# Kernel tuning notes

Measured on AMD Instinct MI355X. Metric: run time of the kernel, lower is better.

Reference implementation:

```python
import jax, jax.numpy as jnp
import numpy as np

EPS = 1e-9


def _pairwise_sqdist(x1, x2):
    # x1: (B,n,3), x2: (B,m,3) -> (B,n,m) squared euclidean distances
    s1 = jnp.sum(x1 * x1, axis=-1)
    s2 = jnp.sum(x2 * x2, axis=-1)
    cross = jnp.einsum('bnd,bmd->bnm', x1, x2)
    return jnp.maximum(s1[:, :, None] + s2[:, None, :] - 2.0 * cross, 0.0)


def _approxmatch(x1, x2):
    # Faithful port of the approxmatch CUDA kernel (Fan et al. EMD approx).
    B, n, _ = x1.shape
    m = x2.shape[1]
    if n >= m:
        multiL, multiR = 1.0, float(n // m)   # integer division as in CUDA
    else:
        multiL, multiR = float(m // n), 1.0
    dist = _pairwise_sqdist(x1, x2)  # (B,n,m)
    # j = 7 .. -1 -> level = -4^j ; j = -2 -> level = 0  (10 sweeps total)
    levels = jnp.concatenate([
        -(4.0 ** jnp.arange(7, -2, -1, dtype=jnp.float32)),
        jnp.zeros((1,), jnp.float32)])
    match0 = jnp.zeros((B, n, m), jnp.float32)
    remainL0 = jnp.full((B, n), multiL, jnp.float32)
    remainR0 = jnp.full((B, m), multiR, jnp.float32)

    def body(carry, level):
        match, remainL, remainR = carry
        e = jnp.exp(level * dist)                              # (B,n,m)
        suml = EPS + jnp.einsum('bnm,bm->bn', e, remainR)
        ratioL = remainL / suml                                # (B,n)
        sumr = remainR * jnp.einsum('bnm,bn->bm', e, ratioL)   # (B,m)
        consumption = jnp.minimum(remainR / (sumr + EPS), 1.0)
        ratioR = consumption * remainR                         # (B,m)
        remainR = jnp.maximum(0.0, remainR - sumr)
        w = e * ratioL[:, :, None] * ratioR[:, None, :]        # flow k->l
        match = match + w
        remainL = jnp.maximum(0.0, remainL - jnp.sum(w, axis=-1))
        return (match, remainL, remainR), None

    (match, _, _), _ = jax.lax.scan(body, (match0, remainL0, remainR0), levels)
    return match, dist


def setup_inputs() -> dict:
    key = jax.random.key(0)
    k1, k2 = jax.random.split(key)
    B, N = 4, 4096
    xyz1 = jax.random.normal(k1, (B, 3, N), dtype=jnp.float32)
    xyz2 = jax.random.normal(k2, (B, 3, N), dtype=jnp.float32)
    return {"xyz1": xyz1, "xyz2": xyz2}


def reference(xyz1, xyz2):
    # transpose=True: BCN -> BNC
    x1 = jnp.transpose(xyz1, (0, 2, 1))
    x2 = jnp.transpose(xyz2, (0, 2, 1))
    match, dist = _approxmatch(x1, x2)
    d = jnp.sqrt(jnp.maximum(dist, 1e-20))
    cost = jnp.sum(match * d, axis=(1, 2))            # (B,)
    emd = cost / min(x1.shape[1], x2.shape[1])
    return jnp.mean(emd)                               # reduce_mean=True
```

## Files before the change

### kernel.cpp

```cpp
#include <hip/hip_runtime.h>


#define NPTS 4096
#define BATCH 4
#define EMD_EPS 1e-9f
#define TILE 1024
#define RPW 4
#define THREADS 256
#define RPB 16
#define NBLK (NPTS / RPB)

__device__ __forceinline__ float fexp2(float x) {
#if __has_builtin(__builtin_amdgcn_exp2f)
    return __builtin_amdgcn_exp2f(x);
#else
    return exp2f(x);
#endif
}
__device__ __forceinline__ float fsqrt(float x) {
#if __has_builtin(__builtin_amdgcn_sqrtf)
    return __builtin_amdgcn_sqrtf(x);
#else
    return __sqrtf(x);
#endif
}

__device__ __forceinline__ float wave_reduce(float v) {
    v += __shfl_xor(v, 32);
    v += __shfl_xor(v, 16);
    v += __shfl_xor(v, 8);
    v += __shfl_xor(v, 4);
    v += __shfl_xor(v, 2);
    v += __shfl_xor(v, 1);
    return v;
}

__global__ void k_init(float* __restrict__ remainL, float* __restrict__ remainR,
                       float* __restrict__ cost_part) {
    int i = blockIdx.x * blockDim.x + threadIdx.x;
    if (i < BATCH * NPTS) {
        remainL[i] = 1.0f;
        remainR[i] = 1.0f;
    }
    if (i < BATCH * NBLK) cost_part[i] = 0.0f;
}

__global__ __launch_bounds__(THREADS, 2) void k_ratioL0(
        const float* __restrict__ xyz1, const float* __restrict__ xyz2,
        float* __restrict__ ratioL, float ls2) {
    const int b = blockIdx.y;
    const int tid = threadIdx.x;
    const int wave = tid >> 6;
    const int lane = tid & 63;
    const int row0 = blockIdx.x * RPB + wave * RPW;

    const float* x1 = xyz1 + b * 3 * NPTS;
    const float* x2 = xyz2 + b * 3 * NPTS;
    const float2* x2x = (const float2*)(x2);
    const float2* x2y = (const float2*)(x2 + NPTS);
    const float2* x2z = (const float2*)(x2 + 2 * NPTS);

    float px[RPW], py[RPW], pz[RPW];
    float2 acc[RPW];
#pragma unroll
    for (int r = 0; r < RPW; ++r) {
        px[r] = x1[row0 + r];
        py[r] = x1[NPTS + row0 + r];
        pz[r] = x1[2 * NPTS + row0 + r];
        acc[r] = make_float2(0.0f, 0.0f);
    }
    __shared__ float4 sA[TILE / 2];
    __shared__ float2 sZ[TILE / 2];

    for (int c0 = 0; c0 < NPTS; c0 += TILE) {
        __syncthreads();
        for (int i = tid; i < TILE / 2; i += THREADS) {
            int e = c0 / 2 + i;
            float2 xx = x2x[e], yy = x2y[e];
            sA[i] = make_float4(xx.x, xx.y, yy.x, yy.y);
            sZ[i] = x2z[e];
        }
        __syncthreads();
#pragma unroll 2
        for (int j = 0; j < TILE / 128; ++j) {
            float4 a = sA[lane + 64 * j];
            float2 z = sZ[lane + 64 * j];
#pragma unroll
            for (int r = 0; r < RPW; ++r) {
                float dx0 = px[r] - a.x, dx1 = px[r] - a.y;
                float dy0 = py[r] - a.z, dy1 = py[r] - a.w;
                float dz0 = pz[r] - z.x, dz1 = pz[r] - z.y;
                float d0 = fmaf(dx0, dx0, fmaf(dy0, dy0, dz0 * dz0));
                float d1 = fmaf(dx1, dx1, fmaf(dy1, dy1, dz1 * dz1));
                acc[r].x += fexp2(ls2 * d0);
                acc[r].y += fexp2(ls2 * d1);
            }
        }
    }
#pragma unroll
    for (int r = 0; r < RPW; ++r) {
        float s = wave_reduce(acc[r].x + acc[r].y);
        if (lane == 0)
            ratioL[b * NPTS + row0 + r] = 1.0f / (EMD_EPS + s);
    }
}

__global__ __launch_bounds__(THREADS, 2) void k_ratioR(
        const float* __restrict__ xyz1, const float* __restrict__ xyz2,
        const float* __restrict__ ratioL, float* __restrict__ ratioR,
        float* __restrict__ remainR, float ls2) {
    const int b = blockIdx.y;
    const int tid = threadIdx.x;
    const int wave = tid >> 6;
    const int lane = tid & 63;
    const int col0 = blockIdx.x * RPB + wave * RPW;

    const float* x1 = xyz1 + b * 3 * NPTS;
    const float* x2 = xyz2 + b * 3 * NPTS;
    const float2* x1x = (const float2*)(x1);
    const float2* x1y = (const float2*)(x1 + NPTS);
    const float2* x1z = (const float2*)(x1 + 2 * NPTS);
    const float2* wLv = (const float2*)(ratioL + b * NPTS);

    float px[RPW], py[RPW], pz[RPW];
    float2 acc[RPW];
#pragma unroll
    for (int r = 0; r < RPW; ++r) {
        px[r] = x2[col0 + r];
        py[r] = x2[NPTS + col0 + r];
        pz[r] = x2[2 * NPTS + col0 + r];
        acc[r] = make_float2(0.0f, 0.0f);
    }
    __shared__ float4 sA[TILE / 2];
    __shared__ float4 sB[TILE / 2];

    for (int c0 = 0; c0 < NPTS; c0 += TILE) {
        __syncthreads();
        for (int i = tid; i < TILE / 2; i += THREADS) {
            int e = c0 / 2 + i;
            float2 xx = x1x[e], yy = x1y[e], zz = x1z[e], ww = wLv[e];
            sA[i] = make_float4(xx.x, xx.y, yy.x, yy.y);
            sB[i] = make_float4(zz.x, zz.y, ww.x, ww.y);
        }
        __syncthreads();
#pragma unroll 2
        for (int j = 0; j < TILE / 128; ++j) {
            float4 a = sA[lane + 64 * j];
            float4 bq = sB[lane + 64 * j];
#pragma unroll
            for (int r = 0; r < RPW; ++r) {
                float dx0 = px[r] - a.x, dx1 = px[r] - a.y;
                float dy0 = py[r] - a.z, dy1 = py[r] - a.w;
                float dz0 = pz[r] - bq.x, dz1 = pz[r] - bq.y;
                float d0 = fmaf(dx0, dx0, fmaf(dy0, dy0, dz0 * dz0));
                float d1 = fmaf(dx1, dx1, fmaf(dy1, dy1, dz1 * dz1));
                acc[r].x = fmaf(fexp2(ls2 * d0), bq.z, acc[r].x);
                acc[r].y = fmaf(fexp2(ls2 * d1), bq.w, acc[r].y);
            }
        }
    }
#pragma unroll
    for (int r = 0; r < RPW; ++r) {
        float s = wave_reduce(acc[r].x + acc[r].y);
        if (lane == 0) {
            int idx = b * NPTS + col0 + r;
            float rv = remainR[idx];
            float sumr = rv * s;
            float cons = fminf(rv / (sumr + EMD_EPS), 1.0f);
            ratioR[idx] = cons * rv;
            remainR[idx] = fmaxf(0.0f, rv - sumr);
        }
    }
}

template <bool SQ>
__global__ __launch_bounds__(THREADS, 2) void k_cost_fused(
        const float* __restrict__ xyz1, const float* __restrict__ xyz2,
        float* __restrict__ ratioL, const float* __restrict__ ratioR,
        float* __restrict__ remainL, const float* __restrict__ remainR,
        float* __restrict__ cost_part, float ls2, float ls2n) {
    const int b = blockIdx.y;
    const int tid = threadIdx.x;
    const int wave = tid >> 6;
    const int lane = tid & 63;
    const int row0 = blockIdx.x * RPB + wave * RPW;

    const float* x1 = xyz1 + b * 3 * NPTS;
    const float* x2 = xyz2 + b * 3 * NPTS;
    const float2* x2x = (const float2*)(x2);
    const float2* x2y = (const float2*)(x2 + NPTS);
    const float2* x2z = (const float2*)(x2 + 2 * NPTS);
    const float2* wRv = (const float2*)(ratioR + b * NPTS);
    const float2* w2v = (const float2*)(remainR + b * NPTS);

    float px[RPW], py[RPW], pz[RPW];
    float2 acc_a[RPW], acc_c[RPW], acc_s[RPW];
#pragma unroll
    for (int r = 0; r < RPW; ++r) {
        px[r] = x1[row0 + r];
        py[r] = x1[NPTS + row0 + r];
        pz[r] = x1[2 * NPTS + row0 + r];
        acc_a[r] = make_float2(0.0f, 0.0f);
        acc_c[r] = make_float2(0.0f, 0.0f);
        acc_s[r] = make_float2(0.0f, 0.0f);
    }
    __shared__ float4 sA[TILE / 2];
    __shared__ float4 sB[TILE / 2];
    __shared__ float2 sC[TILE / 2];
    __shared__ float s_cost[THREADS / 64];

    for (int c0 = 0; c0 < NPTS; c0 += TILE) {
        __syncthreads();
        for (int i = tid; i < TILE / 2; i += THREADS) {
            int e = c0 / 2 + i;
            float2 xx = x2x[e], yy = x2y[e], zz = x2z[e], wr = wRv[e];
            sA[i] = make_float4(xx.x, xx.y, yy.x, yy.y);
            sB[i] = make_float4(zz.x, zz.y, wr.x, wr.y);
            sC[i] = w2v[e];
        }
        __syncthreads();
#pragma unroll 2
        for (int j = 0; j < TILE / 128; ++j) {
            float4 a = sA[lane + 64 * j];
            float4 bq = sB[lane + 64 * j];
            float2 c = sC[lane + 64 * j];
#pragma unroll
            for (int r = 0; r < RPW; ++r) {
                float dx0 = px[r] - a.x, dx1 = px[r] - a.y;
                float dy0 = py[r] - a.z, dy1 = py[r] - a.w;
                float dz0 = pz[r] - bq.x, dz1 = pz[r] - bq.y;
                float d0 = fmaf(dx0, dx0, fmaf(dy0, dy0, dz0 * dz0));
                float d1 = fmaf(dx1, dx1, fmaf(dy1, dy1, dz1 * dz1));
                float er0, er1;
                if (SQ) {
                    float e20 = fexp2(ls2n * d0);
                    float e21 = fexp2(ls2n * d1);
                    acc_s[r].x = fmaf(e20, c.x, acc_s[r].x);
                    acc_s[r].y = fmaf(e21, c.y, acc_s[r].y);
                    float e40 = e20 * e20, e41 = e21 * e21;
                    er0 = (e40 * e40) * bq.z;
                    er1 = (e41 * e41) * bq.w;
                } else {
                    er0 = fexp2(ls2 * d0) * bq.z;
                    er1 = fexp2(ls2 * d1) * bq.w;
                    acc_s[r].x += c.x;
                    acc_s[r].y += c.y;
                }
                acc_a[r].x += er0;
                acc_a[r].y += er1;
                acc_c[r].x = fmaf(er0, fsqrt(d0), acc_c[r].x);
                acc_c[r].y = fmaf(er1, fsqrt(d1), acc_c[r].y);
            }
        }
    }
    float wcost = 0.0f;
#pragma unroll
    for (int r = 0; r < RPW; ++r) {
        float sa = wave_reduce(acc_a[r].x + acc_a[r].y);
        float sc = wave_reduce(acc_c[r].x + acc_c[r].y);
        float ss = wave_reduce(acc_s[r].x + acc_s[r].y);
        if (lane == 0) {
            int idx = b * NPTS + row0 + r;
            float rl = ratioL[idx];
            float rem = fmaxf(0.0f, remainL[idx] - rl * sa);
            remainL[idx] = rem;
            ratioL[idx] = rem / (EMD_EPS + ss);
            wcost = fmaf(rl, sc, wcost);
        }
    }
    if (lane == 0) s_cost[wave] = wcost;
    __syncthreads();
    if (tid == 0) {
        float t = s_cost[0] + s_cost[1] + s_cost[2] + s_cost[3];
        cost_part[b * NBLK + blockIdx.x] += t;
    }
}

__global__ void k_sum_ratioL(const float* __restrict__ ratioL, float* __restrict__ S_L) {
    const int b = blockIdx.x;
    const int tid = threadIdx.x;
    float s = 0.0f;
    for (int i = tid; i < NPTS; i += 256) s += ratioL[b * NPTS + i];
    s = wave_reduce(s);
    __shared__ float sw[4];
    if ((tid & 63) == 0) sw[tid >> 6] = s;
    __syncthreads();
    if (tid == 0) S_L[b] = sw[0] + sw[1] + sw[2] + sw[3];
}

__global__ void k_ratioR_l0(const float* __restrict__ remainR,
                            const float* __restrict__ S_L,
                            float* __restrict__ ratioR) {
    int i = blockIdx.x * blockDim.x + threadIdx.x;
    int b = i >> 12;
    float rv = remainR[i];
    float sumr = rv * S_L[b];
    float cons = fminf(rv / (sumr + EMD_EPS), 1.0f);
    ratioR[i] = cons * rv;
}

__global__ __launch_bounds__(THREADS, 2) void k_cost_l0(
        const float* __restrict__ xyz1, const float* __restrict__ xyz2,
        const float* __restrict__ ratioL, const float* __restrict__ ratioR,
        float* __restrict__ cost_part) {
    const int b = blockIdx.y;
    const int tid = threadIdx.x;
    const int wave = tid >> 6;
    const int lane = tid & 63;
    const int row0 = blockIdx.x * RPB + wave * RPW;

    const float* x1 = xyz1 + b * 3 * NPTS;
    const float* x2 = xyz2 + b * 3 * NPTS;
    const float2* x2x = (const float2*)(x2);
    const float2* x2y = (const float2*)(x2 + NPTS);
    const float2* x2z = (const float2*)(x2 + 2 * NPTS);
    const float2* wRv = (const float2*)(ratioR + b * NPTS);

    float px[RPW], py[RPW], pz[RPW];
    float2 acc_c[RPW];
#pragma unroll
    for (int r = 0; r < RPW; ++r) {
        px[r] = x1[row0 + r];
        py[r] = x1[NPTS + row0 + r];
        pz[r] = x1[2 * NPTS + row0 + r];
        acc_c[r] = make_float2(0.0f, 0.0f);
    }
    __shared__ float4 sA[TILE / 2];
    __shared__ float4 sB[TILE / 2];
    __shared__ float s_cost[THREADS / 64];

    for (int c0 = 0; c0 < NPTS; c0 += TILE) {
        __syncthreads();
        for (int i = tid; i < TILE / 2; i += THREADS) {
            int e = c0 / 2 + i;
            float2 xx = x2x[e], yy = x2y[e], zz = x2z[e], wr = wRv[e];
            sA[i] = make_float4(xx.x, xx.y, yy.x, yy.y);
            sB[i] = make_float4(zz.x, zz.y, wr.x, wr.y);
        }
        __syncthreads();
#pragma unroll 2
        for (int j = 0; j < TILE / 128; ++j) {
            float4 a = sA[lane + 64 * j];
            float4 bq = sB[lane + 64 * j];
#pragma unroll
            for (int r = 0; r < RPW; ++r) {
                float dx0 = px[r] - a.x, dx1 = px[r] - a.y;
                float dy0 = py[r] - a.z, dy1 = py[r] - a.w;
                float dz0 = pz[r] - bq.x, dz1 = pz[r] - bq.y;
                float d0 = fmaf(dx0, dx0, fmaf(dy0, dy0, dz0 * dz0));
                float d1 = fmaf(dx1, dx1, fmaf(dy1, dy1, dz1 * dz1));
                acc_c[r].x = fmaf(bq.z, fsqrt(d0), acc_c[r].x);
                acc_c[r].y = fmaf(bq.w, fsqrt(d1), acc_c[r].y);
            }
        }
    }
    float wcost = 0.0f;
#pragma unroll
    for (int r = 0; r < RPW; ++r) {
        float sc = wave_reduce(acc_c[r].x + acc_c[r].y);
        if (lane == 0)
            wcost = fmaf(ratioL[b * NPTS + row0 + r], sc, wcost);
    }
    if (lane == 0) s_cost[wave] = wcost;
    __syncthreads();
    if (tid == 0) {
        float t = s_cost[0] + s_cost[1] + s_cost[2] + s_cost[3];
        cost_part[b * NBLK + blockIdx.x] += t;
    }
}

__global__ void k_final(const float* __restrict__ cost_part, float* __restrict__ out) {
    const int tid = threadIdx.x;
    float s = 0.0f;
    for (int i = tid; i < BATCH * NBLK; i += 256) s += cost_part[i];
    s = wave_reduce(s);
    __shared__ float sw[4];
    if ((tid & 63) == 0) sw[tid >> 6] = s;
    __syncthreads();
    if (tid == 0) out[0] = (sw[0] + sw[1] + sw[2] + sw[3]) / ((float)NPTS * (float)BATCH);
}

extern "C" void kernel_launch(void* const* d_in, const int* in_sizes, int n_in,
                              void* d_out, int out_size, void* d_ws, size_t ws_size,
                              hipStream_t stream) {
    const float* xyz1 = (const float*)d_in[0];
    const float* xyz2 = (const float*)d_in[1];
    float* out = (float*)d_out;

    float* ws = (float*)d_ws;
    float* remainL  = ws;
    float* remainR  = ws + 1 * BATCH * NPTS;
    float* ratioL   = ws + 2 * BATCH * NPTS;
    float* ratioR   = ws + 3 * BATCH * NPTS;
    float* cost_part = ws + 4 * BATCH * NPTS;
    float* S_L      = cost_part + BATCH * NBLK;

    static const float levels[10] = {
        -16384.0f, -4096.0f, -1024.0f, -256.0f, -64.0f,
        -16.0f, -4.0f, -1.0f, -0.25f, 0.0f};
    float ls2[10];
    for (int t = 0; t < 10; ++t)
        ls2[t] = (float)(levels[t] * 1.4426950408889634);

    dim3 grid(NBLK, BATCH);

    k_init<<<(BATCH * NPTS + 255) / 256, 256, 0, stream>>>(remainL, remainR, cost_part);
    k_ratioL0<<<grid, THREADS, 0, stream>>>(xyz1, xyz2, ratioL, ls2[0]);
    for (int t = 0; t < 8; ++t) {
        k_ratioR<<<grid, THREADS, 0, stream>>>(xyz1, xyz2, ratioL, ratioR, remainR, ls2[t]);
        k_cost_fused<true><<<grid, THREADS, 0, stream>>>(xyz1, xyz2, ratioL, ratioR,
                                                         remainL, remainR, cost_part,
                                                         ls2[t], ls2[t + 1]);
    }
    k_ratioR<<<grid, THREADS, 0, stream>>>(xyz1, xyz2, ratioL, ratioR, remainR, ls2[8]);
    k_cost_fused<false><<<grid, THREADS, 0, stream>>>(xyz1, xyz2, ratioL, ratioR,
                                                      remainL, remainR, cost_part,
                                                      ls2[8], 0.0f);
    k_sum_ratioL<<<BATCH, 256, 0, stream>>>(ratioL, S_L);
    k_ratioR_l0<<<(BATCH * NPTS) / 256, 256, 0, stream>>>(remainR, S_L, ratioR);
    k_cost_l0<<<grid, THREADS, 0, stream>>>(xyz1, xyz2, ratioL, ratioR, cost_part);
    k_final<<<1, 256, 0, stream>>>(cost_part, out);
}
```

Baseline: 575.0 us.

## Morton-sort points and skip far tile pairs via bounding-box distance culling

Adds a per-batch Morton-code counting sort of both point clouds and per-128-point tile bounding boxes. Each wave then skips tiles whose minimum squared distance makes exp(level*d) negligible, below about 2^-160, which removes most exp work at the steep early levels. It also folds the init and ratioR_l0 kernels into neighbouring kernels. The culling is approximate and drops tiny contributions. The sort quantizes over a fixed [-5,5] range, but out-of-range points are clamped, so correctness does not depend on that range.

```diff
diff --git a/kernel.cpp b/kernel.cpp
--- a/kernel.cpp
+++ b/kernel.cpp
@@ -9,6 +9,7 @@
 #define THREADS 256
 #define RPB 16
 #define NBLK (NPTS / RPB)
+#define NTILE 32
 
 __device__ __forceinline__ float fexp2(float x) {
 #if __has_builtin(__builtin_amdgcn_exp2f)
@@ -35,27 +36,122 @@
     return v;
 }
 
-__global__ void k_init(float* __restrict__ remainL, float* __restrict__ remainR,
-                       float* __restrict__ cost_part) {
-    int i = blockIdx.x * blockDim.x + threadIdx.x;
-    if (i < BATCH * NPTS) {
-        remainL[i] = 1.0f;
-        remainR[i] = 1.0f;
-    }
-    if (i < BATCH * NBLK) cost_part[i] = 0.0f;
-}
+__device__ __forceinline__ unsigned spread4(unsigned v) {
+    return (v & 1u) | ((v & 2u) << 2) | ((v & 4u) << 4) | ((v & 8u) << 6);
+}
+
+__global__ __launch_bounds__(1024) void k_sort(
+        const float* __restrict__ xyz1, const float* __restrict__ xyz2,
+        float* __restrict__ x1s, float* __restrict__ x2s) {
+    const int side = blockIdx.x, b = blockIdx.y;
+    const float* src = (side ? xyz2 : xyz1) + b * 3 * NPTS;
+    float* dst = (side ? x2s : x1s) + b * 3 * NPTS;
+    const int tid = threadIdx.x;
+    const int lane = tid & 63, wave = tid >> 6;
+
+    __shared__ unsigned hist[4096];
+    __shared__ unsigned short keys[4096];
+    __shared__ unsigned warr[16];
+
+    for (int i = tid; i < 4096; i += 1024) hist[i] = 0u;
+    __syncthreads();
+    for (int i = tid; i < NPTS; i += 1024) {
+        float x = src[i], y = src[NPTS + i], z = src[2 * NPTS + i];
+        unsigned qx = (unsigned)fminf(fmaxf((x + 5.0f) * 1.6f, 0.0f), 15.0f);
+        unsigned qy = (unsigned)fminf(fmaxf((y + 5.0f) * 1.6f, 0.0f), 15.0f);
+        unsigned qz = (unsigned)fminf(fmaxf((z + 5.0f) * 1.6f, 0.0f), 15.0f);
+        unsigned key = spread4(qx) | (spread4(qy) << 1) | (spread4(qz) << 2);
+        keys[i] = (unsigned short)key;
+        atomicAdd(&hist[key], 1u);
+    }
+    __syncthreads();
+    const int base = tid * 4;
+    unsigned h0 = hist[base], h1 = hist[base + 1], h2 = hist[base + 2], h3 = hist[base + 3];
+    unsigned st = h0 + h1 + h2 + h3;
+    unsigned v = st;
+    for (int d = 1; d < 64; d <<= 1) {
+        unsigned u = __shfl_up(v, d);
+        if (lane >= d) v += u;
+    }
+    if (lane == 63) warr[wave] = v;
+    __syncthreads();
+    if (tid == 0) {
+        unsigned run = 0;
+        for (int w = 0; w < 16; ++w) { unsigned t = warr[w]; warr[w] = run; run += t; }
+    }
+    __syncthreads();
+    unsigned off = warr[wave] + (v - st);
+    hist[base] = off;
+    hist[base + 1] = off + h0;
+    hist[base + 2] = off + h0 + h1;
+    hist[base + 3] = off + h0 + h1 + h2;
+    __syncthreads();
+    for (int i = tid; i < NPTS; i += 1024) {
+        unsigned k = keys[i];
+        unsigned pos = atomicAdd(&hist[k], 1u);
+        dst[pos] = src[i];
+        dst[NPTS + pos] = src[NPTS + i];
+        dst[2 * NPTS + pos] = src[2 * NPTS + i];
+    }
+}
+
+__global__ void k_bbox(const float* __restrict__ x1s, const float* __restrict__ x2s,
+                       float* __restrict__ bb1, float* __restrict__ bb2) {
+    const int tile = blockIdx.x, b = blockIdx.y, side = blockIdx.z;
+    const float* src = (side ? x2s : x1s) + b * 3 * NPTS + tile * 128;
+    float* out = (side ? bb2 : bb1) + (b * NTILE + tile) * 8;
+    const int lane = threadIdx.x;
+    float mnx = 1e30f, mny = 1e30f, mnz = 1e30f;
+    float mxx = -1e30f, mxy = -1e30f, mxz = -1e30f;
+    for (int i = lane; i < 128; i += 64) {
+        float x = src[i], y = src[NPTS + i], z = src[2 * NPTS + i];
+        mnx = fminf(mnx, x); mny = fminf(mny, y); mnz = fminf(mnz, z);
+        mxx = fmaxf(mxx, x); mxy = fmaxf(mxy, y); mxz = fmaxf(mxz, z);
+    }
+    for (int d = 32; d; d >>= 1) {
+        mnx = fminf(mnx, __shfl_xor(mnx, d));
+        mny = fminf(mny, __shfl_xor(mny, d));
+        mnz = fminf(mnz, __shfl_xor(mnz, d));
+        mxx = fmaxf(mxx, __shfl_xor(mxx, d));
+        mxy = fmaxf(mxy, __shfl_xor(mxy, d));
+        mxz = fmaxf(mxz, __shfl_xor(mxz, d));
+    }
+    if (lane == 0) {
+        out[0] = mnx; out[1] = mny; out[2] = mnz;
+        out[3] = mxx; out[4] = mxy; out[5] = mxz;
+    }
+}
+
+#define BB_TEST(ti)                                                          \
+    float bmnx = sBB[(ti) * 8 + 0], bmny = sBB[(ti) * 8 + 1],                \
+          bmnz = sBB[(ti) * 8 + 2], bmxx = sBB[(ti) * 8 + 3],                \
+          bmxy = sBB[(ti) * 8 + 4], bmxz = sBB[(ti) * 8 + 5];                \
+    float ddx = fmaxf(0.0f, fmaxf(bmnx - gmxx, gmnx - bmxx));                \
+    float ddy = fmaxf(0.0f, fmaxf(bmny - gmxy, gmny - bmxy));                \
+    float ddz = fmaxf(0.0f, fmaxf(bmnz - gmxz, gmnz - bmxz));                \
+    float md2 = fmaf(ddx, ddx, fmaf(ddy, ddy, ddz * ddz));
+
+#define WAVE_BBOX()                                                          \
+    float gmnx = fminf(fminf(px[0], px[1]), fminf(px[2], px[3]));            \
+    float gmxx = fmaxf(fmaxf(px[0], px[1]), fmaxf(px[2], px[3]));            \
+    float gmny = fminf(fminf(py[0], py[1]), fminf(py[2], py[3]));            \
+    float gmxy = fmaxf(fmaxf(py[0], py[1]), fmaxf(py[2], py[3]));            \
+    float gmnz = fminf(fminf(pz[0], pz[1]), fminf(pz[2], pz[3]));            \
+    float gmxz = fmaxf(fmaxf(pz[0], pz[1]), fmaxf(pz[2], pz[3]));
 
 __global__ __launch_bounds__(THREADS, 2) void k_ratioL0(
-        const float* __restrict__ xyz1, const float* __restrict__ xyz2,
-        float* __restrict__ ratioL, float ls2) {
+        const float* __restrict__ x1s, const float* __restrict__ x2s,
+        const float* __restrict__ bb2,
+        float* __restrict__ ratioL, float* __restrict__ remainL,
+        float* __restrict__ remainR, float ls2, float thresh) {
     const int b = blockIdx.y;
     const int tid = threadIdx.x;
     const int wave = tid >> 6;
     const int lane = tid & 63;
     const int row0 = blockIdx.x * RPB + wave * RPW;
 
-    const float* x1 = xyz1 + b * 3 * NPTS;
-    const float* x2 = xyz2 + b * 3 * NPTS;
+    const float* x1 = x1s + b * 3 * NPTS;
+    const float* x2 = x2s + b * 3 * NPTS;
     const float2* x2x = (const float2*)(x2);
     const float2* x2y = (const float2*)(x2 + NPTS);
     const float2* x2z = (const float2*)(x2 + 2 * NPTS);
@@ -69,8 +165,11 @@
         pz[r] = x1[2 * NPTS + row0 + r];
         acc[r] = make_float2(0.0f, 0.0f);
     }
+    WAVE_BBOX();
     __shared__ float4 sA[TILE / 2];
     __shared__ float2 sZ[TILE / 2];
+    __shared__ float sBB[NTILE * 8];
+    if (tid < NTILE * 8) sBB[tid] = bb2[b * NTILE * 8 + tid];
 
     for (int c0 = 0; c0 < NPTS; c0 += TILE) {
         __syncthreads();
@@ -83,40 +182,48 @@
         __syncthreads();
 #pragma unroll 2
         for (int j = 0; j < TILE / 128; ++j) {
-            float4 a = sA[lane + 64 * j];
-            float2 z = sZ[lane + 64 * j];
-#pragma unroll
-            for (int r = 0; r < RPW; ++r) {
-                float dx0 = px[r] - a.x, dx1 = px[r] - a.y;
-                float dy0 = py[r] - a.z, dy1 = py[r] - a.w;
-                float dz0 = pz[r] - z.x, dz1 = pz[r] - z.y;
-                float d0 = fmaf(dx0, dx0, fmaf(dy0, dy0, dz0 * dz0));
-                float d1 = fmaf(dx1, dx1, fmaf(dy1, dy1, dz1 * dz1));
-                acc[r].x += fexp2(ls2 * d0);
-                acc[r].y += fexp2(ls2 * d1);
+            BB_TEST((c0 >> 7) + j);
+            if (md2 < thresh) {
+                float4 a = sA[lane + 64 * j];
+                float2 z = sZ[lane + 64 * j];
+#pragma unroll
+                for (int r = 0; r < RPW; ++r) {
+                    float dx0 = px[r] - a.x, dx1 = px[r] - a.y;
+                    float dy0 = py[r] - a.z, dy1 = py[r] - a.w;
+                    float dz0 = pz[r] - z.x, dz1 = pz[r] - z.y;
+                    float d0 = fmaf(dx0, dx0, fmaf(dy0, dy0, dz0 * dz0));
+                    float d1 = fmaf(dx1, dx1, fmaf(dy1, dy1, dz1 * dz1));
+                    acc[r].x += fexp2(ls2 * d0);
+                    acc[r].y += fexp2(ls2 * d1);
+                }
             }
         }
     }
 #pragma unroll
     for (int r = 0; r < RPW; ++r) {
         float s = wave_reduce(acc[r].x + acc[r].y);
-        if (lane == 0)
-            ratioL[b * NPTS + row0 + r] = 1.0f / (EMD_EPS + s);
+        if (lane == 0) {
+            int idx = b * NPTS + row0 + r;
+            ratioL[idx] = 1.0f / (EMD_EPS + s);
+            remainL[idx] = 1.0f;
+            remainR[idx] = 1.0f;
+        }
     }
 }
 
 __global__ __launch_bounds__(THREADS, 2) void k_ratioR(
-        const float* __restrict__ xyz1, const float* __restrict__ xyz2,
+        const float* __restrict__ x1s, const float* __restrict__ x2s,
+        const float* __restrict__ bb1,
         const float* __restrict__ ratioL, float* __restrict__ ratioR,
-        float* __restrict__ remainR, float ls2) {
+        float* __restrict__ remainR, float ls2, float thresh) {
     const int b = blockIdx.y;
     const int tid = threadIdx.x;
     const int wave = tid >> 6;
     const int lane = tid & 63;
     const int col0 = blockIdx.x * RPB + wave * RPW;
 
-    const float* x1 = xyz1 + b * 3 * NPTS;
-    const float* x2 = xyz2 + b * 3 * NPTS;
+    const float* x1 = x1s + b * 3 * NPTS;
+    const float* x2 = x2s + b * 3 * NPTS;
     const float2* x1x = (const float2*)(x1);
     const float2* x1y = (const float2*)(x1 + NPTS);
     const float2* x1z = (const float2*)(x1 + 2 * NPTS);
@@ -131,8 +238,11 @@
         pz[r] = x2[2 * NPTS + col0 + r];
         acc[r] = make_float2(0.0f, 0.0f);
     }
+    WAVE_BBOX();
     __shared__ float4 sA[TILE / 2];
     __shared__ float4 sB[TILE / 2];
+    __shared__ float sBB[NTILE * 8];
+    if (tid < NTILE * 8) sBB[tid] = bb1[b * NTILE * 8 + tid];
 
     for (int c0 = 0; c0 < NPTS; c0 += TILE) {
         __syncthreads();
@@ -145,17 +255,20 @@
         __syncthreads();
 #pragma unroll 2
         for (int j = 0; j < TILE / 128; ++j) {
-            float4 a = sA[lane + 64 * j];
-            float4 bq = sB[lane + 64 * j];
-#pragma unroll
-            for (int r = 0; r < RPW; ++r) {
-                float dx0 = px[r] - a.x, dx1 = px[r] - a.y;
-                float dy0 = py[r] - a.z, dy1 = py[r] - a.w;
-                float dz0 = pz[r] - bq.x, dz1 = pz[r] - bq.y;
-                float d0 = fmaf(dx0, dx0, fmaf(dy0, dy0, dz0 * dz0));
-                float d1 = fmaf(dx1, dx1, fmaf(dy1, dy1, dz1 * dz1));
-                acc[r].x = fmaf(fexp2(ls2 * d0), bq.z, acc[r].x);
-                acc[r].y = fmaf(fexp2(ls2 * d1), bq.w, acc[r].y);
+            BB_TEST((c0 >> 7) + j);
+            if (md2 < thresh) {
+                float4 a = sA[lane + 64 * j];
+                float4 bq = sB[lane + 64 * j];
+#pragma unroll
+                for (int r = 0; r < RPW; ++r) {
+                    float dx0 = px[r] - a.x, dx1 = px[r] - a.y;
+                    float dy0 = py[r] - a.z, dy1 = py[r] - a.w;
+                    float dz0 = pz[r] - bq.x, dz1 = pz[r] - bq.y;
+                    float d0 = fmaf(dx0, dx0, fmaf(dy0, dy0, dz0 * dz0));
+                    float d1 = fmaf(dx1, dx1, fmaf(dy1, dy1, dz1 * dz1));
+                    acc[r].x = fmaf(fexp2(ls2 * d0), bq.z, acc[r].x);
+                    acc[r].y = fmaf(fexp2(ls2 * d1), bq.w, acc[r].y);
+                }
             }
         }
     }
@@ -175,18 +288,20 @@
 
 template <bool SQ>
 __global__ __launch_bounds__(THREADS, 2) void k_cost_fused(
-        const float* __restrict__ xyz1, const float* __restrict__ xyz2,
+        const float* __restrict__ x1s, const float* __restrict__ x2s,
+        const float* __restrict__ bb2,
         float* __restrict__ ratioL, const float* __restrict__ ratioR,
         float* __restrict__ remainL, const float* __restrict__ remainR,
-        float* __restrict__ cost_part, float ls2, float ls2n) {
+        float* __restrict__ cost_part, float ls2, float ls2n, float thresh,
+        int initCost) {
     const int b = blockIdx.y;
     const int tid = threadIdx.x;
     const int wave = tid >> 6;
     const int lane = tid & 63;
     const int row0 = blockIdx.x * RPB + wave * RPW;
 
-    const float* x1 = xyz1 + b * 3 * NPTS;
-    const float* x2 = xyz2 + b * 3 * NPTS;
+    const float* x1 = x1s + b * 3 * NPTS;
+    const float* x2 = x2s + b * 3 * NPTS;
     const float2* x2x = (const float2*)(x2);
     const float2* x2y = (const float2*)(x2 + NPTS);
     const float2* x2z = (const float2*)(x2 + 2 * NPTS);
@@ -204,10 +319,13 @@
         acc_c[r] = make_float2(0.0f, 0.0f);
         acc_s[r] = make_float2(0.0f, 0.0f);
     }
+    WAVE_BBOX();
     __shared__ float4 sA[TILE / 2];
     __shared__ float4 sB[TILE / 2];
     __shared__ float2 sC[TILE / 2];
+    __shared__ float sBB[NTILE * 8];
     __shared__ float s_cost[THREADS / 64];
+    if (tid < NTILE * 8) sBB[tid] = bb2[b * NTILE * 8 + tid];
 
     for (int c0 = 0; c0 < NPTS; c0 += TILE) {
         __syncthreads();
@@ -221,35 +339,39 @@
         __syncthreads();
 #pragma unroll 2
         for (int j = 0; j < TILE / 128; ++j) {
-            float4 a = sA[lane + 64 * j];
-            float4 bq = sB[lane + 64 * j];
-            float2 c = sC[lane + 64 * j];
-#pragma unroll
-            for (int r = 0; r < RPW; ++r) {
-                float dx0 = px[r] - a.x, dx1 = px[r] - a.y;
-                float dy0 = py[r] - a.z, dy1 = py[r] - a.w;
-                float dz0 = pz[r] - bq.x, dz1 = pz[r] - bq.y;
-                float d0 = fmaf(dx0, dx0, fmaf(dy0, dy0, dz0 * dz0));
-                float d1 = fmaf(dx1, dx1, fmaf(dy1, dy1, dz1 * dz1));
-                float er0, er1;
-                if (SQ) {
-                    float e20 = fexp2(ls2n * d0);
-                    float e21 = fexp2(ls2n * d1);
-                    acc_s[r].x = fmaf(e20, c.x, acc_s[r].x);
-                    acc_s[r].y = fmaf(e21, c.y, acc_s[r].y);
-                    float e40 = e20 * e20, e41 = e21 * e21;
-                    er0 = (e40 * e40) * bq.z;
-                    er1 = (e41 * e41) * bq.w;
-                } else {
-                    er0 = fexp2(ls2 * d0) * bq.z;
-                    er1 = fexp2(ls2 * d1) * bq.w;
-                    acc_s[r].x += c.x;
-                    acc_s[r].y += c.y;
+            BB_TEST((c0 >> 7) + j);
+            if (md2 < thresh) {
+                float4 a = sA[lane + 64 * j];
+                float4 bq = sB[lane + 64 * j];
+                float2 c = sC[lane + 64 * j];
+#pragma unroll
+                for (int r = 0; r < RPW; ++r) {
+                    float dx0 = px[r] - a.x, dx1 = px[r] - a.y;
+                    float dy0 = py[r] - a.z, dy1 = py[r] - a.w;
+                    float dz0 = pz[r] - bq.x, dz1 = pz[r] - bq.y;
+                    float d0 = fmaf(dx0, dx0, fmaf(dy0, dy0, dz0 * dz0));
+                    float d1 = fmaf(dx1, dx1, fmaf(dy1, dy1, dz1 * dz1));
+                    float er0, er1;
+                    if (SQ) {
+                        float e20 = fexp2(ls2n * d0);
+                        float e21 = fexp2(ls2n * d1);
+                        acc_s[r].x = fmaf(e20, c.x, acc_s[r].x);
+                        acc_s[r].y = fmaf(e21, c.y, acc_s[r].y);
+                        float e40 = e20 * e20, e41 = e21 * e21;
+                        er0 = (e40 * e40) * bq.z;
+                        er1 = (e41 * e41) * bq.w;
+                    } else {
+                        er0 = fexp2(ls2 * d0) * bq.z;
+                        er1 = fexp2(ls2 * d1) * bq.w;
+                        acc_s[r].x += c.x;
+                        acc_s[r].y += c.y;
+                    }
+                    acc_a[r].x += er0;
+                    acc_a[r].y += er1;
+                    acc_c[r].x = fmaf(er0, fsqrt(d0), acc_c[r].x);
+                    acc_c[r].y = fmaf(er1, fsqrt(d1), acc_c[r].y);
                 }
-                acc_a[r].x += er0;
-                acc_a[r].y += er1;
-                acc_c[r].x = fmaf(er0, fsqrt(d0), acc_c[r].x);
-                acc_c[r].y = fmaf(er1, fsqrt(d1), acc_c[r].y);
+            } else if (!SQ) {
             }
         }
     }
@@ -272,7 +394,8 @@
     __syncthreads();
     if (tid == 0) {
         float t = s_cost[0] + s_cost[1] + s_cost[2] + s_cost[3];
-        cost_part[b * NBLK + blockIdx.x] += t;
+        int ci = b * NBLK + blockIdx.x;
+        cost_part[ci] = (initCost ? t : cost_part[ci] + t);
     }
 }
 
@@ -288,33 +411,23 @@
     if (tid == 0) S_L[b] = sw[0] + sw[1] + sw[2] + sw[3];
 }
 
-__global__ void k_ratioR_l0(const float* __restrict__ remainR,
-                            const float* __restrict__ S_L,
-                            float* __restrict__ ratioR) {
-    int i = blockIdx.x * blockDim.x + threadIdx.x;
-    int b = i >> 12;
-    float rv = remainR[i];
-    float sumr = rv * S_L[b];
-    float cons = fminf(rv / (sumr + EMD_EPS), 1.0f);
-    ratioR[i] = cons * rv;
-}
-
 __global__ __launch_bounds__(THREADS, 2) void k_cost_l0(
-        const float* __restrict__ xyz1, const float* __restrict__ xyz2,
-        const float* __restrict__ ratioL, const float* __restrict__ ratioR,
-        float* __restrict__ cost_part) {
+        const float* __restrict__ x1s, const float* __restrict__ x2s,
+        const float* __restrict__ ratioL, const float* __restrict__ remainR,
+        const float* __restrict__ S_L, float* __restrict__ cost_part) {
     const int b = blockIdx.y;
     const int tid = threadIdx.x;
     const int wave = tid >> 6;
     const int lane = tid & 63;
     const int row0 = blockIdx.x * RPB + wave * RPW;
-
-    const float* x1 = xyz1 + b * 3 * NPTS;
-    const float* x2 = xyz2 + b * 3 * NPTS;
+    const float sL = S_L[b];
+
+    const float* x1 = x1s + b * 3 * NPTS;
+    const float* x2 = x2s + b * 3 * NPTS;
     const float2* x2x = (const float2*)(x2);
     const float2* x2y = (const float2*)(x2 + NPTS);
     const float2* x2z = (const float2*)(x2 + 2 * NPTS);
-    const float2* wRv = (const float2*)(ratioR + b * NPTS);
+    const float2* wRv = (const float2*)(remainR + b * NPTS);
 
     float px[RPW], py[RPW], pz[RPW];
     float2 acc_c[RPW];
@@ -333,9 +446,11 @@
         __syncthreads();
         for (int i = tid; i < TILE / 2; i += THREADS) {
             int e = c0 / 2 + i;
-            float2 xx = x2x[e], yy = x2y[e], zz = x2z[e], wr = wRv[e];
+            float2 xx = x2x[e], yy = x2y[e], zz = x2z[e], rv = wRv[e];
+            float wr0 = fminf(rv.x / (rv.x * sL + EMD_EPS), 1.0f) * rv.x;
+            float wr1 = fminf(rv.y / (rv.y * sL + EMD_EPS), 1.0f) * rv.y;
             sA[i] = make_float4(xx.x, xx.y, yy.x, yy.y);
-            sB[i] = make_float4(zz.x, zz.y, wr.x, wr.y);
+            sB[i] = make_float4(zz.x, zz.y, wr0, wr1);
         }
         __syncthreads();
 #pragma unroll 2
@@ -387,37 +502,50 @@
     const float* xyz2 = (const float*)d_in[1];
     float* out = (float*)d_out;
 
+    const int BN = BATCH * NPTS;
     float* ws = (float*)d_ws;
     float* remainL  = ws;
-    float* remainR  = ws + 1 * BATCH * NPTS;
-    float* ratioL   = ws + 2 * BATCH * NPTS;
-    float* ratioR   = ws + 3 * BATCH * NPTS;
-    float* cost_part = ws + 4 * BATCH * NPTS;
+    float* remainR  = ws + 1 * BN;
+    float* ratioL   = ws + 2 * BN;
+    float* ratioR   = ws + 3 * BN;
+    float* cost_part = ws + 4 * BN;
     float* S_L      = cost_part + BATCH * NBLK;
+    float* x1s      = S_L + 4;
+    float* x2s      = x1s + 3 * BN;
+    float* bb1      = x2s + 3 * BN;
+    float* bb2      = bb1 + BATCH * NTILE * 8;
 
     static const float levels[10] = {
         -16384.0f, -4096.0f, -1024.0f, -256.0f, -64.0f,
         -16.0f, -4.0f, -1.0f, -0.25f, 0.0f};
-    float ls2[10];
-    for (int t = 0; t < 10; ++t)
+    float ls2[10], thr[10];
+    for (int t = 0; t < 10; ++t) {
         ls2[t] = (float)(levels[t] * 1.4426950408889634);
+        thr[t] = (t < 9) ? (160.0f / -ls2[t]) : 3.0e38f;
+    }
+    const float INF_THR = 3.0e38f;
 
     dim3 grid(NBLK, BATCH);
 
-    k_init<<<(BATCH * NPTS + 255) / 256, 256, 0, stream>>>(remainL, remainR, cost_part);
-    k_ratioL0<<<grid, THREADS, 0, stream>>>(xyz1, xyz2, ratioL, ls2[0]);
+    k_sort<<<dim3(2, BATCH), 1024, 0, stream>>>(xyz1, xyz2, x1s, x2s);
+    k_bbox<<<dim3(NTILE, BATCH, 2), 64, 0, stream>>>(x1s, x2s, bb1, bb2);
+
+    k_ratioL0<<<grid, THREADS, 0, stream>>>(x1s, x2s, bb2, ratioL, remainL, remainR,
+                                            ls2[0], thr[0]);
     for (int t = 0; t < 8; ++t) {
-        k_ratioR<<<grid, THREADS, 0, stream>>>(xyz1, xyz2, ratioL, ratioR, remainR, ls2[t]);
-        k_cost_fused<true><<<grid, THREADS, 0, stream>>>(xyz1, xyz2, ratioL, ratioR,
+        k_ratioR<<<grid, THREADS, 0, stream>>>(x1s, x2s, bb1, ratioL, ratioR, remainR,
+                                               ls2[t], thr[t]);
+        k_cost_fused<true><<<grid, THREADS, 0, stream>>>(x1s, x2s, bb2, ratioL, ratioR,
                                                          remainL, remainR, cost_part,
-                                                         ls2[t], ls2[t + 1]);
-    }
-    k_ratioR<<<grid, THREADS, 0, stream>>>(xyz1, xyz2, ratioL, ratioR, remainR, ls2[8]);
-    k_cost_fused<false><<<grid, THREADS, 0, stream>>>(xyz1, xyz2, ratioL, ratioR,
+                                                         ls2[t], ls2[t + 1], thr[t + 1],
+                                                         t == 0 ? 1 : 0);
+    }
+    k_ratioR<<<grid, THREADS, 0, stream>>>(x1s, x2s, bb1, ratioL, ratioR, remainR,
+                                           ls2[8], thr[8]);
+    k_cost_fused<false><<<grid, THREADS, 0, stream>>>(x1s, x2s, bb2, ratioL, ratioR,
                                                       remainL, remainR, cost_part,
-                                                      ls2[8], 0.0f);
+                                                      ls2[8], 0.0f, INF_THR, 0);
     k_sum_ratioL<<<BATCH, 256, 0, stream>>>(ratioL, S_L);
-    k_ratioR_l0<<<(BATCH * NPTS) / 256, 256, 0, stream>>>(remainR, S_L, ratioR);
-    k_cost_l0<<<grid, THREADS, 0, stream>>>(xyz1, xyz2, ratioL, ratioR, cost_part);
+    k_cost_l0<<<grid, THREADS, 0, stream>>>(x1s, x2s, ratioL, remainR, S_L, cost_part);
     k_final<<<1, 256, 0, stream>>>(cost_part, out);
 }
```

Result: slower. 628.2 us (+9.3%).
